# Optimization experiments

Measured on AMD Instinct MI355X. Metric: run time of the kernel, lower is better.

Reference implementation:

```python
import jax, jax.numpy as jnp
import numpy as np

N = 16384      # total atoms (8 proteins x ~2048)
E = 524288     # N * max_neighbors(32)
B = 8          # graphs
F_IN = 26      # 20 residue types + 6 atom types
D = 128        # node_dim
H = 256        # hidden_dim
OUT = 64       # output_dim
L = 4          # n_layers
N_RBF = 16
CUTOFF = 10.0


def setup_inputs() -> dict:
    key = jax.random.key(0)
    ks = jax.random.split(key, 24)
    s = 0.05
    inp = {
        "positions": jax.random.normal(ks[0], (N, 3), jnp.float32) * 10.0,
        "node_features": jax.random.normal(ks[1], (N, F_IN), jnp.float32),
        "edge_index": jax.random.randint(ks[2], (2, E), 0, N, jnp.int32),
        "batch": jnp.sort(jax.random.randint(ks[3], (N,), 0, B, jnp.int32)),
        # node embedding MLP
        "emb_W1": jax.random.normal(ks[4], (F_IN, D), jnp.float32) * s,
        "emb_b1": jnp.zeros((D,), jnp.float32),
        "emb_W2": jax.random.normal(ks[5], (D, D), jnp.float32) * s,
        "emb_b2": jnp.zeros((D,), jnp.float32),
        # per-layer message MLP: [2D + n_rbf] -> H -> D
        "msg_W1": jax.random.normal(ks[6], (L, 2 * D + N_RBF, H), jnp.float32) * s,
        "msg_b1": jnp.zeros((L, H), jnp.float32),
        "msg_W2": jax.random.normal(ks[7], (L, H, D), jnp.float32) * s,
        "msg_b2": jnp.zeros((L, D), jnp.float32),
        # per-layer update MLP: [2D] -> H -> D (residual)
        "upd_W1": jax.random.normal(ks[8], (L, 2 * D, H), jnp.float32) * s,
        "upd_b1": jnp.zeros((L, H), jnp.float32),
        "upd_W2": jax.random.normal(ks[9], (L, H, D), jnp.float32) * s,
        "upd_b2": jnp.zeros((L, D), jnp.float32),
        # readout MLP: D -> H -> OUT
        "r_W1": jax.random.normal(ks[10], (D, H), jnp.float32) * s,
        "r_b1": jnp.zeros((H,), jnp.float32),
        "r_W2": jax.random.normal(ks[11], (H, OUT), jnp.float32) * s,
        "r_b2": jnp.zeros((OUT,), jnp.float32),
    }
    return inp


def _mlp2(x, W1, b1, W2, b2):
    return jax.nn.silu(x @ W1 + b1) @ W2 + b2


def _edge_rbf(positions, src, dst):
    rel = positions[dst] - positions[src]                      # (E,3)
    d = jnp.sqrt(jnp.sum(rel * rel, axis=-1) + 1e-12)          # (E,)
    centers = jnp.linspace(0.0, CUTOFF, N_RBF, dtype=positions.dtype)
    width = CUTOFF / N_RBF
    rbf = jnp.exp(-((d[:, None] - centers) ** 2) / (2.0 * width * width))  # (E,n_rbf)
    env = 0.5 * (jnp.cos(jnp.pi * d / CUTOFF) + 1.0) * (d < CUTOFF)        # cosine cutoff
    return rbf * env[:, None]


def reference(positions, node_features, edge_index, batch,
              emb_W1, emb_b1, emb_W2, emb_b2,
              msg_W1, msg_b1, msg_W2, msg_b2,
              upd_W1, upd_b1, upd_W2, upd_b2,
              r_W1, r_b1, r_W2, r_b2):
    src, dst = edge_index[0], edge_index[1]
    h = _mlp2(node_features, emb_W1, emb_b1, emb_W2, emb_b2)   # (N,D)
    ef = _edge_rbf(positions, src, dst)                        # (E,n_rbf)
    for i in range(L):
        m_in = jnp.concatenate([h[src], h[dst], ef], axis=-1)  # (E,2D+n_rbf)
        m = _mlp2(m_in, msg_W1[i], msg_b1[i], msg_W2[i], msg_b2[i])  # (E,D)
        agg = jax.ops.segment_sum(m, dst, num_segments=N)      # (N,D)
        u_in = jnp.concatenate([h, agg], axis=-1)              # (N,2D)
        h = h + _mlp2(u_in, upd_W1[i], upd_b1[i], upd_W2[i], upd_b2[i])
    # mean readout per graph
    counts = jax.ops.segment_sum(jnp.ones((N,), h.dtype), batch, num_segments=B)
    g = jax.ops.segment_sum(h, batch, num_segments=B) / jnp.maximum(counts, 1.0)[:, None]
    return _mlp2(g, r_W1, r_b1, r_W2, r_b2)                    # (B,OUT)
```

## Files before the change

kernel.cpp:

```cpp
#include <hip/hip_runtime.h>
#include <math.h>

#define NATOMS 16384
#define NEDGES 524288
#define NLAYERS 4
#define TE 64

typedef __bf16 bf16x8 __attribute__((ext_vector_type(8)));
typedef __bf16 bf16x4 __attribute__((ext_vector_type(4)));
typedef __bf16 bf16x2 __attribute__((ext_vector_type(2)));
typedef float f32x4 __attribute__((ext_vector_type(4)));

__device__ __forceinline__ float silu_f(float x) {
  return x * __builtin_amdgcn_rcpf(1.0f + __expf(-x));
}

__global__ __launch_bounds__(1024) void scan_kernel(
    const int* __restrict__ counts, int* __restrict__ cursor,
    float* __restrict__ degf)
{
  __shared__ int s_tot[1024];
  int tid = threadIdx.x;
  int v[16];
  {
    const int4* cp = (const int4*)(counts + tid * 16);
    int4 a = cp[0], b = cp[1], c = cp[2], d = cp[3];
    v[0]=a.x; v[1]=a.y; v[2]=a.z; v[3]=a.w;
    v[4]=b.x; v[5]=b.y; v[6]=b.z; v[7]=b.w;
    v[8]=c.x; v[9]=c.y; v[10]=c.z; v[11]=c.w;
    v[12]=d.x; v[13]=d.y; v[14]=d.z; v[15]=d.w;
  }
  int tot = 0;
  #pragma unroll
  for (int i = 0; i < 16; i++) tot += v[i];
  s_tot[tid] = tot;
  __syncthreads();
  for (int off = 1; off < 1024; off <<= 1) {
    int t = (tid >= off) ? s_tot[tid - off] : 0;
    __syncthreads();
    s_tot[tid] += t;
    __syncthreads();
  }
  int run = s_tot[tid] - tot;
  #pragma unroll
  for (int i = 0; i < 16; i++) {
    cursor[tid * 16 + i] = run;
    degf[tid * 16 + i] = (float)v[i];
    run += v[i];
  }
}

__global__ __launch_bounds__(256) void scatter_rbf_kernel(
    const int* __restrict__ src, const int* __restrict__ dst,
    int* __restrict__ cursor, const float* __restrict__ pos,
    int* __restrict__ esrc, int* __restrict__ edst,
    __bf16* __restrict__ efb)
{
  int e = blockIdx.x * 256 + threadIdx.x;
  int s = src[e], d = dst[e];
  int p = atomicAdd(&cursor[d], 1);
  esrc[p] = s;
  edst[p] = d;
  float dx = pos[d * 3 + 0] - pos[s * 3 + 0];
  float dy = pos[d * 3 + 1] - pos[s * 3 + 1];
  float dz = pos[d * 3 + 2] - pos[s * 3 + 2];
  float dist = sqrtf(dx * dx + dy * dy + dz * dz + 1e-12f);
  float env = (dist < 10.0f)
                  ? 0.5f * (cosf(3.14159265358979f * dist * 0.1f) + 1.0f)
                  : 0.0f;
  bf16x8 o0, o1;
  #pragma unroll
  for (int i = 0; i < 16; i++) {
    float c = (10.0f / 15.0f) * (float)i;
    float t = dist - c;
    float v = env * __expf(-t * t * 1.28f);
    if (i < 8) o0[i] = (__bf16)v; else o1[i - 8] = (__bf16)v;
  }
  *(bf16x8*)(efb + (size_t)p * 16 + 0) = o0;
  *(bf16x8*)(efb + (size_t)p * 16 + 8) = o1;
}

#define NB_PREP (801 * NLAYERS)
#define NB_HIST (NEDGES / 256)
#define NB_EMB  (NATOMS / 2)

__global__ __launch_bounds__(256) void front_kernel(
    const float* __restrict__ mW1, const float* __restrict__ mW2,
    const float* __restrict__ uW1, const float* __restrict__ uW2,
    const float* __restrict__ mb2,
    __bf16* __restrict__ W1at, __bf16* __restrict__ W1bt,
    __bf16* __restrict__ B2c, __bf16* __restrict__ uW1ft,
    __bf16* __restrict__ uW2t, float* __restrict__ b2u,
    const int* __restrict__ dstI, int* __restrict__ counts,
    const float* __restrict__ x, const float* __restrict__ eW1,
    const float* __restrict__ eb1, const float* __restrict__ eW2,
    const float* __restrict__ eb2, float* __restrict__ h,
    __bf16* __restrict__ hb)
{
  __shared__ float xs[2][26];
  __shared__ float hid[2][132];
  int bxf = blockIdx.x, tid = threadIdx.x;

  if (bxf < NB_PREP) {
    long l = bxf / 801;
    int bx = bxf - (int)l * 801;
    if (bx < 128) {
      int i = bx * 256 + tid;
      int n = i >> 7, k = i & 127;
      W1at[l * (256L * 128) + i] = (__bf16)mW1[l * (272L * 256) + (size_t)k * 256 + n];
    } else if (bx < 256) {
      int i = (bx - 128) * 256 + tid;
      int n = i >> 7, k = i & 127;
      W1bt[l * (256L * 128) + i] = (__bf16)mW1[l * (272L * 256) + (size_t)(128 + k) * 256 + n];
    } else if (bx < 288) {
      int i = (bx - 256) * 256 + tid;
      int c = i >> 5, k = i & 31;
      float v = (k < 16) ? mW1[l * (272L * 256) + (size_t)(256 + k) * 256 + c] : 0.0f;
      B2c[l * (256L * 32) + i] = (__bf16)v;
    } else if (bx < 672) {
      int k = bx - 288;
      int n = tid;
      float v;
      if (k < 128) {
        v = uW1[l * 65536 + (size_t)k * 256 + n];
      } else {
        int r = k - 128;
        v = 0.0f;
        for (int j = 0; j < 128; j++)
          v += mW2[(l * 256 + r) * 128 + j] * uW1[l * 65536 + (size_t)(128 + j) * 256 + n];
      }
      uW1ft[l * (256L * 384) + (size_t)n * 384 + k] = (__bf16)v;
    } else if (bx < 800) {
      int i = (bx - 672) * 256 + tid;
      int n = i >> 8, k = i & 255;
      uW2t[l * (128L * 256) + i] = (__bf16)uW2[l * (256L * 128) + (size_t)k * 128 + n];
    } else {
      int c = tid;
      float acc = 0.0f;
      for (int j = 0; j < 128; j++)
        acc += mb2[l * 128 + j] * uW1[l * 65536 + (size_t)(128 + j) * 256 + c];
      b2u[l * 256 + c] = acc;
    }
  } else if (bxf < NB_PREP + NB_HIST) {
    int e = (bxf - NB_PREP) * 256 + tid;
    atomicAdd(&counts[dstI[e]], 1);
  } else {
    int nb = bxf - (NB_PREP + NB_HIST);
    int hf = tid >> 7, j = tid & 127;
    int n = nb * 2 + hf;
    if (j < 26) xs[hf][j] = x[(size_t)n * 26 + j];
    __syncthreads();
    float acc = eb1[j];
    #pragma unroll
    for (int k = 0; k < 26; k++) acc += xs[hf][k] * eW1[k * 128 + j];
    hid[hf][j] = silu_f(acc);
    __syncthreads();
    float acc2 = eb2[j];
    #pragma unroll 8
    for (int k = 0; k < 128; k++) acc2 += hid[hf][k] * eW2[k * 128 + j];
    h[(size_t)n * 128 + j] = acc2;
    hb[(size_t)n * 128 + j] = (__bf16)acc2;
  }
}

__global__ __launch_bounds__(256) void zprep_kernel(
    const __bf16* __restrict__ hb, const float* __restrict__ b1,
    const __bf16* __restrict__ W1at, const __bf16* __restrict__ W1bt,
    __bf16* __restrict__ z1b, __bf16* __restrict__ z2b, float* __restrict__ aggH)
{
  __shared__ __bf16 s_n[64][136];
  int tid = threadIdx.x, n0 = blockIdx.x * 64;
  {
    int n = tid >> 2, t4 = tid & 3;
    const bf16x8* hr = (const bf16x8*)(hb + (size_t)(n0 + n) * 128);
    #pragma unroll
    for (int i = 0; i < 4; i++)
      *(bf16x8*)&s_n[n][t4 * 8 + 32 * i] = hr[t4 + 4 * i];
  }
  {
    float4 zz = make_float4(0.f, 0.f, 0.f, 0.f);
    float4* ap = (float4*)(aggH + (size_t)n0 * 256);
    for (int i = tid; i < 64 * 256 / 4; i += 256) ap[i] = zz;
  }
  __syncthreads();
  const int wv = tid >> 6, ln = tid & 63, lc = ln & 15, qd = ln >> 4;
  for (int cp = 0; cp < 2; cp++) {
    f32x4 aA[4][2], aB[4][2];
    #pragma unroll
    for (int nt = 0; nt < 2; nt++) {
      float bv = b1[cp * 128 + wv * 32 + nt * 16 + lc];
      #pragma unroll
      for (int mt = 0; mt < 4; mt++) {
        aA[mt][nt][0] = 0.f; aA[mt][nt][1] = 0.f;
        aA[mt][nt][2] = 0.f; aA[mt][nt][3] = 0.f;
        aB[mt][nt][0] = bv; aB[mt][nt][1] = bv;
        aB[mt][nt][2] = bv; aB[mt][nt][3] = bv;
      }
    }
    #pragma unroll
    for (int kt = 0; kt < 4; kt++) {
      bf16x8 af[4];
      #pragma unroll
      for (int mt = 0; mt < 4; mt++)
        af[mt] = *(const bf16x8*)&s_n[mt * 16 + lc][kt * 32 + qd * 8];
      bf16x8 bwA[2], bwB[2];
      #pragma unroll
      for (int nt = 0; nt < 2; nt++) {
        int c = cp * 128 + wv * 32 + nt * 16 + lc;
        bwA[nt] = *(const bf16x8*)(W1at + (size_t)c * 128 + kt * 32 + qd * 8);
        bwB[nt] = *(const bf16x8*)(W1bt + (size_t)c * 128 + kt * 32 + qd * 8);
      }
      #pragma unroll
      for (int mt = 0; mt < 4; mt++)
        #pragma unroll
        for (int nt = 0; nt < 2; nt++) {
          aA[mt][nt] = __builtin_amdgcn_mfma_f32_16x16x32_bf16(af[mt], bwA[nt], aA[mt][nt], 0, 0, 0);
          aB[mt][nt] = __builtin_amdgcn_mfma_f32_16x16x32_bf16(af[mt], bwB[nt], aB[mt][nt], 0, 0, 0);
        }
    }
    #pragma unroll
    for (int mt = 0; mt < 4; mt++)
      #pragma unroll
      for (int nt = 0; nt < 2; nt++) {
        int c = cp * 128 + wv * 32 + nt * 16 + lc;
        #pragma unroll
        for (int r = 0; r < 4; r++) {
          int n = n0 + mt * 16 + qd * 4 + r;
          z1b[(size_t)n * 256 + c] = (__bf16)aA[mt][nt][r];
          z2b[(size_t)n * 256 + c] = (__bf16)aB[mt][nt][r];
        }
      }
  }
}

__global__ __launch_bounds__(256, 7) void msg_mfma_kernel(
    const __bf16* __restrict__ z1b, const __bf16* __restrict__ z2b,
    const __bf16* __restrict__ efb,
    const int* __restrict__ esrc, const int* __restrict__ edst,
    const __bf16* __restrict__ B2c, float* __restrict__ aggH)
{
  __shared__ __align__(16) __bf16 s_hT[128][70];
  __shared__ __align__(16) __bf16 s_ef[TE][24];
  __shared__ int s_src[TE];
  __shared__ int s_dst[TE];
  __shared__ unsigned int s_mask[2];

  int tid = threadIdx.x, e0 = blockIdx.x * TE;

  if (tid < TE) {
    int d = edst[e0 + tid];
    s_dst[tid] = d;
    int dp = (tid == 0) ? (d ^ 1) : edst[e0 + tid - 1];
    unsigned long long mb = __ballot(d != dp);
    if (tid == 0) { s_mask[0] = (unsigned int)mb; s_mask[1] = (unsigned int)(mb >> 32); }
  } else if (tid < 2 * TE) {
    s_src[tid - TE] = esrc[e0 + tid - TE];
  }
  {
    int e = tid >> 2, t4 = tid & 3;
    if (t4 < 2)
      *(bf16x8*)&s_ef[e][t4 * 8] =
          *(const bf16x8*)(efb + (size_t)(e0 + e) * 16 + t4 * 8);
  }
  __syncthreads();

  const int wv = tid >> 6, ln = tid & 63, lc = ln & 15, qd = ln >> 4;

  bf16x8 bI;
  #pragma unroll
  for (int j = 0; j < 8; j++)
    bI[j] = (__bf16)((lc == (qd & 1) * 8 + j) ? 1.0f : 0.0f);

  const __bf16* pz[4];
  #pragma unroll
  for (int mt = 0; mt < 4; mt++) {
    int m = mt * 16 + lc;
    int row = (qd < 2) ? s_src[m] : s_dst[m];
    pz[mt] = ((qd < 2) ? z1b : z2b) + (size_t)row * 256 + (qd & 1) * 8;
  }

  bf16x8 aef[4];
  #pragma unroll
  for (int mt = 0; mt < 4; mt++)
    aef[mt] = *(const bf16x8*)&s_ef[mt * 16 + lc][(qd & 1) * 8];

  const int sj = tid & 127;
  const int srow0 = (tid >> 7) * 32;
  const unsigned int smask = __builtin_amdgcn_readfirstlane(s_mask[tid >> 7]);

  #pragma unroll
  for (int hf = 0; hf < 2; hf++) {
    if (hf) __syncthreads();

    #pragma unroll
    for (int nt = 0; nt < 2; nt++) {
      const int cb = hf * 128 + wv * 32 + nt * 16;
      bf16x8 bw = *(const bf16x8*)(B2c + (size_t)(cb + lc) * 32 + qd * 8);
      #pragma unroll
      for (int mt = 0; mt < 4; mt++) {
        bf16x8 az = *(const bf16x8*)(pz[mt] + cb);
        f32x4 z; z[0] = 0.f; z[1] = 0.f; z[2] = 0.f; z[3] = 0.f;
        f32x4 acc = __builtin_amdgcn_mfma_f32_16x16x32_bf16(az, bI, z, 0, 0, 0);
        acc = __builtin_amdgcn_mfma_f32_16x16x32_bf16(aef[mt], bw, acc, 0, 0, 0);
        bf16x2 p0, p1;
        p0[0] = (__bf16)silu_f(acc[0]); p0[1] = (__bf16)silu_f(acc[1]);
        p1[0] = (__bf16)silu_f(acc[2]); p1[1] = (__bf16)silu_f(acc[3]);
        __bf16* wp = &s_hT[wv * 32 + nt * 16 + lc][mt * 16 + qd * 4];
        *(bf16x2*)wp = p0;
        *(bf16x2*)(wp + 2) = p1;
      }
    }
    __syncthreads();

    {
      const int gcol = hf * 128 + sj;
      float acc = 0.0f;
      int cur = s_dst[srow0];
      #pragma unroll 8
      for (int i = 0; i < 32; i += 2) {
        bf16x2 p = *(const bf16x2*)&s_hT[sj][srow0 + i];
        if (i > 0 && ((smask >> i) & 1u)) {
          atomicAdd(&aggH[(size_t)cur * 256 + gcol], acc);
          acc = 0.0f; cur = s_dst[srow0 + i];
        }
        acc += (float)p[0];
        if ((smask >> (i + 1)) & 1u) {
          atomicAdd(&aggH[(size_t)cur * 256 + gcol], acc);
          acc = 0.0f; cur = s_dst[srow0 + i + 1];
        }
        acc += (float)p[1];
      }
      atomicAdd(&aggH[(size_t)cur * 256 + gcol], acc);
    }
  }
}

__global__ __launch_bounds__(512, 2) void upd_mfma_kernel(
    float* __restrict__ h, __bf16* __restrict__ hb,
    float* __restrict__ aggH, const float* __restrict__ degf,
    const __bf16* __restrict__ uW1ft, const float* __restrict__ b1,
    const float* __restrict__ b2u,
    const __bf16* __restrict__ uW2t, const float* __restrict__ b2,
    int do_z, const float* __restrict__ nb1,
    const __bf16* __restrict__ nW1at, const __bf16* __restrict__ nW1bt,
    __bf16* __restrict__ z1b, __bf16* __restrict__ z2b)
{
  __shared__ __bf16 s_u[64][392];
  __shared__ __bf16 s_uh[64][264];
  int tid = threadIdx.x, n0 = blockIdx.x * 64;
  {
    int n = tid >> 3, t8 = tid & 7;
    const bf16x8* hr = (const bf16x8*)(hb + (size_t)(n0 + n) * 128);
    #pragma unroll
    for (int i = 0; i < 2; i++)
      *(bf16x8*)&s_u[n][t8 * 8 + 64 * i] = hr[t8 + 8 * i];
    const float* sr = aggH + (size_t)(n0 + n) * 256;
    #pragma unroll
    for (int i = 0; i < 4; i++) {
      int col = t8 * 8 + i * 64;
      float4 a = *(const float4*)(sr + col);
      float4 b = *(const float4*)(sr + col + 4);
      bf16x8 o;
      o[0] = (__bf16)a.x; o[1] = (__bf16)a.y; o[2] = (__bf16)a.z; o[3] = (__bf16)a.w;
      o[4] = (__bf16)b.x; o[5] = (__bf16)b.y; o[6] = (__bf16)b.z; o[7] = (__bf16)b.w;
      *(bf16x8*)&s_u[n][128 + col] = o;
    }
  }
  __syncthreads();
  const int wv = tid >> 6, ln = tid & 63, lc = ln & 15, qd = ln >> 4;

  float dg[4][4];
  #pragma unroll
  for (int mt = 0; mt < 4; mt++)
    #pragma unroll
    for (int r = 0; r < 4; r++)
      dg[mt][r] = degf[n0 + mt * 16 + qd * 4 + r];

  {
    f32x4 acc1[4][2];
    #pragma unroll
    for (int nt = 0; nt < 2; nt++) {
      int c = wv * 32 + nt * 16 + lc;
      float bv = b1[c];
      float b2uv = b2u[c];
      #pragma unroll
      for (int mt = 0; mt < 4; mt++)
        #pragma unroll
        for (int r = 0; r < 4; r++)
          acc1[mt][nt][r] = bv + dg[mt][r] * b2uv;
    }
    #pragma unroll
    for (int kt = 0; kt < 12; kt++) {
      bf16x8 af[4];
      #pragma unroll
      for (int mt = 0; mt < 4; mt++)
        af[mt] = *(const bf16x8*)&s_u[mt * 16 + lc][kt * 32 + qd * 8];
      bf16x8 bw[2];
      #pragma unroll
      for (int nt = 0; nt < 2; nt++)
        bw[nt] = *(const bf16x8*)(uW1ft +
                 (size_t)(wv * 32 + nt * 16 + lc) * 384 + kt * 32 + qd * 8);
      #pragma unroll
      for (int mt = 0; mt < 4; mt++)
        #pragma unroll
        for (int nt = 0; nt < 2; nt++)
          acc1[mt][nt] = __builtin_amdgcn_mfma_f32_16x16x32_bf16(af[mt], bw[nt], acc1[mt][nt], 0, 0, 0);
    }
    #pragma unroll
    for (int mt = 0; mt < 4; mt++)
      #pragma unroll
      for (int nt = 0; nt < 2; nt++) {
        int cc = wv * 32 + nt * 16 + lc;
        #pragma unroll
        for (int r = 0; r < 4; r++)
          s_uh[mt * 16 + qd * 4 + r][cc] = (__bf16)silu_f(acc1[mt][nt][r]);
      }
  }
  __syncthreads();

  const int ow = wv * 16 + lc;
  f32x4 acc2[4];
  {
    float bv = b2[ow];
    #pragma unroll
    for (int mt = 0; mt < 4; mt++) {
      acc2[mt][0] = bv; acc2[mt][1] = bv; acc2[mt][2] = bv; acc2[mt][3] = bv;
    }
  }
  #pragma unroll
  for (int kt = 0; kt < 8; kt++) {
    bf16x8 a2[4];
    #pragma unroll
    for (int mt = 0; mt < 4; mt++)
      a2[mt] = *(const bf16x8*)&s_uh[mt * 16 + lc][kt * 32 + qd * 8];
    bf16x8 b2w = *(const bf16x8*)(uW2t + (size_t)ow * 256 + kt * 32 + qd * 8);
    #pragma unroll
    for (int mt = 0; mt < 4; mt++)
      acc2[mt] = __builtin_amdgcn_mfma_f32_16x16x32_bf16(a2[mt], b2w, acc2[mt], 0, 0, 0);
  }

  #pragma unroll
  for (int mt = 0; mt < 4; mt++)
    #pragma unroll
    for (int r = 0; r < 4; r++) {
      int n = n0 + mt * 16 + qd * 4 + r;
      float v = h[(size_t)n * 128 + ow] + acc2[mt][r];
      h[(size_t)n * 128 + ow] = v;
      hb[(size_t)n * 128 + ow] = (__bf16)v;
    }

  if (do_z) {
    __syncthreads();
    {
      float4 zz = make_float4(0.f, 0.f, 0.f, 0.f);
      float4* ap = (float4*)(aggH + (size_t)n0 * 256);
      for (int i = tid; i < 64 * 256 / 4; i += 512) ap[i] = zz;
      int n = tid >> 3, t8 = tid & 7;
      const bf16x8* hr = (const bf16x8*)(hb + (size_t)(n0 + n) * 128);
      #pragma unroll
      for (int i = 0; i < 2; i++)
        *(bf16x8*)&s_u[n][t8 * 8 + 64 * i] = hr[t8 + 8 * i];
    }
    __syncthreads();
    f32x4 aA[4][2], aB[4][2];
    #pragma unroll
    for (int nt = 0; nt < 2; nt++) {
      float bv = nb1[wv * 32 + nt * 16 + lc];
      #pragma unroll
      for (int mt = 0; mt < 4; mt++) {
        aA[mt][nt][0] = 0.f; aA[mt][nt][1] = 0.f;
        aA[mt][nt][2] = 0.f; aA[mt][nt][3] = 0.f;
        aB[mt][nt][0] = bv; aB[mt][nt][1] = bv;
        aB[mt][nt][2] = bv; aB[mt][nt][3] = bv;
      }
    }
    #pragma unroll
    for (int kt = 0; kt < 4; kt++) {
      bf16x8 af[4];
      #pragma unroll
      for (int mt = 0; mt < 4; mt++)
        af[mt] = *(const bf16x8*)&s_u[mt * 16 + lc][kt * 32 + qd * 8];
      bf16x8 bwA[2], bwB[2];
      #pragma unroll
      for (int nt = 0; nt < 2; nt++) {
        int c = wv * 32 + nt * 16 + lc;
        bwA[nt] = *(const bf16x8*)(nW1at + (size_t)c * 128 + kt * 32 + qd * 8);
        bwB[nt] = *(const bf16x8*)(nW1bt + (size_t)c * 128 + kt * 32 + qd * 8);
      }
      #pragma unroll
      for (int mt = 0; mt < 4; mt++)
        #pragma unroll
        for (int nt = 0; nt < 2; nt++) {
          aA[mt][nt] = __builtin_amdgcn_mfma_f32_16x16x32_bf16(af[mt], bwA[nt], aA[mt][nt], 0, 0, 0);
          aB[mt][nt] = __builtin_amdgcn_mfma_f32_16x16x32_bf16(af[mt], bwB[nt], aB[mt][nt], 0, 0, 0);
        }
    }
    #pragma unroll
    for (int mt = 0; mt < 4; mt++)
      #pragma unroll
      for (int nt = 0; nt < 2; nt++) {
        int c = wv * 32 + nt * 16 + lc;
        #pragma unroll
        for (int r = 0; r < 4; r++) {
          int n = n0 + mt * 16 + qd * 4 + r;
          z1b[(size_t)n * 256 + c] = (__bf16)aA[mt][nt][r];
          z2b[(size_t)n * 256 + c] = (__bf16)aB[mt][nt][r];
        }
      }
  }
}

__global__ __launch_bounds__(128) void readout_sum_kernel(
    const float* __restrict__ h, const int* __restrict__ batch,
    float* __restrict__ gsum, float* __restrict__ gcnt)
{
  int j = threadIdx.x;
  int n0 = blockIdx.x * 128;
  float acc = 0.f, cacc = 0.f;
  int cur = batch[n0];
  for (int i = 0; i < 128; i++) {
    int b = batch[n0 + i];
    if (b != cur) {
      atomicAdd(&gsum[cur * 128 + j], acc);
      if (j == 0) atomicAdd(&gcnt[cur], cacc);
      acc = 0.f; cacc = 0.f; cur = b;
    }
    acc += h[(size_t)(n0 + i) * 128 + j];
    cacc += 1.f;
  }
  atomicAdd(&gsum[cur * 128 + j], acc);
  if (j == 0) atomicAdd(&gcnt[cur], cacc);
}

__global__ __launch_bounds__(256) void readout_mlp_kernel(
    const float* __restrict__ gsum, const float* __restrict__ gcnt,
    const float* __restrict__ W1, const float* __restrict__ b1,
    const float* __restrict__ W2, const float* __restrict__ b2,
    float* __restrict__ out)
{
  __shared__ float g[8][128];
  __shared__ float hid[8][256];
  int tid = threadIdx.x;
  for (int i = tid; i < 8 * 128; i += 256) {
    int b = i >> 7, c = i & 127;
    g[b][c] = gsum[i] / fmaxf(gcnt[b], 1.0f);
  }
  __syncthreads();
  {
    float bb = b1[tid];
    float a[8];
    #pragma unroll
    for (int b = 0; b < 8; b++) a[b] = bb;
    for (int k = 0; k < 128; k++) {
      float w = W1[k * 256 + tid];
      #pragma unroll
      for (int b = 0; b < 8; b++) a[b] += g[b][k] * w;
    }
    #pragma unroll
    for (int b = 0; b < 8; b++) hid[b][tid] = silu_f(a[b]);
  }
  __syncthreads();
  int j = tid & 63, bg = tid >> 6;
  float a0 = b2[j], a1 = b2[j];
  for (int k = 0; k < 256; k++) {
    float w = W2[k * 64 + j];
    a0 += hid[bg * 2 + 0][k] * w;
    a1 += hid[bg * 2 + 1][k] * w;
  }
  out[(bg * 2 + 0) * 64 + j] = a0;
  out[(bg * 2 + 1) * 64 + j] = a1;
}

extern "C" void kernel_launch(void* const* d_in, const int* in_sizes, int n_in,
                              void* d_out, int out_size, void* d_ws, size_t ws_size,
                              hipStream_t stream) {
  const float* pos   = (const float*)d_in[0];
  const float* xfeat = (const float*)d_in[1];
  const int*   eidx  = (const int*)d_in[2];
  const int*   batch = (const int*)d_in[3];
  const float* eW1 = (const float*)d_in[4];
  const float* eb1 = (const float*)d_in[5];
  const float* eW2 = (const float*)d_in[6];
  const float* eb2 = (const float*)d_in[7];
  const float* mW1 = (const float*)d_in[8];
  const float* mb1 = (const float*)d_in[9];
  const float* mW2 = (const float*)d_in[10];
  const float* mb2 = (const float*)d_in[11];
  const float* uW1 = (const float*)d_in[12];
  const float* ub1 = (const float*)d_in[13];
  const float* uW2 = (const float*)d_in[14];
  const float* ub2 = (const float*)d_in[15];
  const float* rW1 = (const float*)d_in[16];
  const float* rb1 = (const float*)d_in[17];
  const float* rW2 = (const float*)d_in[18];
  const float* rb2 = (const float*)d_in[19];

  const int* srcI = eidx;
  const int* dstI = eidx + NEDGES;

  char* base = (char*)d_ws;
  float* h    = (float*)base;  base += (size_t)NATOMS * 128 * 4;
  float* aggH = (float*)base;  base += (size_t)NATOMS * 256 * 4;
  __bf16* z1b = (__bf16*)base; base += (size_t)NATOMS * 256 * 2;
  __bf16* z2b = (__bf16*)base; base += (size_t)NATOMS * 256 * 2;
  __bf16* hb  = (__bf16*)base; base += (size_t)NATOMS * 128 * 2;
  __bf16* efb = (__bf16*)base; base += (size_t)NEDGES * 16 * 2;
  __bf16* W1at = (__bf16*)base; base += (size_t)NLAYERS * 256 * 128 * 2;
  __bf16* W1bt = (__bf16*)base; base += (size_t)NLAYERS * 256 * 128 * 2;
  __bf16* B2c  = (__bf16*)base; base += (size_t)NLAYERS * 256 * 32 * 2;
  __bf16* uW1ft = (__bf16*)base; base += (size_t)NLAYERS * 256 * 384 * 2;
  __bf16* uW2t = (__bf16*)base; base += (size_t)NLAYERS * 128 * 256 * 2;
  float* b2u  = (float*)base;  base += (size_t)NLAYERS * 256 * 4;
  float* degf = (float*)base;  base += (size_t)NATOMS * 4;
  float* gsum = (float*)base;  base += 8 * 128 * 4;
  float* gcnt = (float*)base;  base += 8 * 4;
  int* counts = (int*)base;    base += (size_t)NATOMS * 4;
  int* cursor = (int*)base;    base += (size_t)NATOMS * 4;
  int* esrc   = (int*)base;    base += (size_t)NEDGES * 4;
  int* edst   = (int*)base;    base += (size_t)NEDGES * 4;

  hipMemsetAsync(counts, 0, NATOMS * sizeof(int), stream);

  front_kernel<<<NB_PREP + NB_HIST + NB_EMB, 256, 0, stream>>>(
      mW1, mW2, uW1, uW2, mb2, W1at, W1bt, B2c, uW1ft, uW2t, b2u,
      dstI, counts, xfeat, eW1, eb1, eW2, eb2, h, hb);

  scan_kernel<<<1, 1024, 0, stream>>>(counts, cursor, degf);
  scatter_rbf_kernel<<<NEDGES / 256, 256, 0, stream>>>(
      srcI, dstI, cursor, pos, esrc, edst, efb);

  zprep_kernel<<<NATOMS / 64, 256, 0, stream>>>(
      hb, mb1, W1at, W1bt, z1b, z2b, aggH);

  for (int l = 0; l < NLAYERS; l++) {
    int ln = (l < NLAYERS - 1) ? (l + 1) : l;
    msg_mfma_kernel<<<NEDGES / TE, 256, 0, stream>>>(
        z1b, z2b, efb, esrc, edst,
        B2c + (size_t)l * 256 * 32, aggH);
    upd_mfma_kernel<<<NATOMS / 64, 512, 0, stream>>>(
        h, hb, aggH, degf,
        uW1ft + (size_t)l * 256 * 384, ub1 + (size_t)l * 256,
        b2u + (size_t)l * 256,
        uW2t + (size_t)l * 128 * 256, ub2 + (size_t)l * 128,
        (l < NLAYERS - 1) ? 1 : 0,
        mb1 + (size_t)ln * 256,
        W1at + (size_t)ln * 256 * 128, W1bt + (size_t)ln * 256 * 128,
        z1b, z2b);
  }

  hipMemsetAsync(gsum, 0, (8 * 128 + 8) * sizeof(float), stream);
  readout_sum_kernel<<<NATOMS / 128, 128, 0, stream>>>(h, batch, gsum, gcnt);
  readout_mlp_kernel<<<1, 256, 0, stream>>>(gsum, gcnt, rW1, rb1, rW2, rb2,
                                            (float*)d_out);
}
```

Measured before the change: 599.2 us.

## Tile weight transposes through LDS and batch embedding MLP over 32 atoms per block

Weight-preparation blocks now transpose 64x64 tiles through shared memory, so both the reads and the bf16 writes are coalesced, instead of doing strided per-element gathers. The folded mW2*uW1 product is computed 16 rows per block with register accumulators, which cuts the number of prep blocks per layer from 801 to 50. The node embedding MLP now handles 32 atoms per block, with each thread keeping 16 accumulators so every weight load is reused across atoms. The cost is more register pressure and a larger shared-memory footprint per block, in exchange for fewer blocks and far less redundant global traffic.

```diff
diff --git a/kernel.cpp b/kernel.cpp
--- a/kernel.cpp
+++ b/kernel.cpp
@@ -80,9 +80,10 @@
   *(bf16x8*)(efb + (size_t)p * 16 + 8) = o1;
 }
 
-#define NB_PREP (801 * NLAYERS)
+#define NB_PL   50
+#define NB_PREP (NB_PL * NLAYERS)
 #define NB_HIST (NEDGES / 256)
-#define NB_EMB  (NATOMS / 2)
+#define NB_EMB  (NATOMS / 32)
 
 __global__ __launch_bounds__(256) void front_kernel(
     const float* __restrict__ mW1, const float* __restrict__ mW2,
@@ -97,69 +98,156 @@
     const float* __restrict__ eb2, float* __restrict__ h,
     __bf16* __restrict__ hb)
 {
-  __shared__ float xs[2][26];
-  __shared__ float hid[2][132];
+  __shared__ __align__(16) char smem[19712];
   int bxf = blockIdx.x, tid = threadIdx.x;
 
   if (bxf < NB_PREP) {
-    long l = bxf / 801;
-    int bx = bxf - (int)l * 801;
-    if (bx < 128) {
-      int i = bx * 256 + tid;
-      int n = i >> 7, k = i & 127;
-      W1at[l * (256L * 128) + i] = (__bf16)mW1[l * (272L * 256) + (size_t)k * 256 + n];
-    } else if (bx < 256) {
-      int i = (bx - 128) * 256 + tid;
-      int n = i >> 7, k = i & 127;
-      W1bt[l * (256L * 128) + i] = (__bf16)mW1[l * (272L * 256) + (size_t)(128 + k) * 256 + n];
-    } else if (bx < 288) {
-      int i = (bx - 256) * 256 + tid;
-      int c = i >> 5, k = i & 31;
-      float v = (k < 16) ? mW1[l * (272L * 256) + (size_t)(256 + k) * 256 + c] : 0.0f;
-      B2c[l * (256L * 32) + i] = (__bf16)v;
-    } else if (bx < 672) {
-      int k = bx - 288;
-      int n = tid;
-      float v;
-      if (k < 128) {
-        v = uW1[l * 65536 + (size_t)k * 256 + n];
-      } else {
-        int r = k - 128;
-        v = 0.0f;
-        for (int j = 0; j < 128; j++)
-          v += mW2[(l * 256 + r) * 128 + j] * uW1[l * 65536 + (size_t)(128 + j) * 256 + n];
-      }
-      uW1ft[l * (256L * 384) + (size_t)n * 384 + k] = (__bf16)v;
-    } else if (bx < 800) {
-      int i = (bx - 672) * 256 + tid;
-      int n = i >> 8, k = i & 255;
-      uW2t[l * (128L * 256) + i] = (__bf16)uW2[l * (256L * 128) + (size_t)k * 128 + n];
+    int l = bxf / NB_PL;
+    int bx = bxf - l * NB_PL;
+    if (bx < 16) {
+      float (*tile)[65] = (float(*)[65])smem;
+      int tt = bx & 7;
+      int row0 = ((tt >> 2) * 64) + ((bx < 8) ? 0 : 128);
+      int col0 = (tt & 3) * 64;
+      const float* Sp = mW1 + (size_t)l * (272 * 256) + (size_t)row0 * 256 + col0;
+      __bf16* Dq = ((bx < 8) ? W1at : W1bt) + (size_t)l * (256 * 128);
+      int dro = (bx < 8) ? row0 : row0 - 128;
+      int c = tid & 63, r4 = tid >> 6;
+      #pragma unroll
+      for (int i = 0; i < 16; i++)
+        tile[r4 + i * 4][c] = Sp[(size_t)(r4 + i * 4) * 256 + c];
+      __syncthreads();
+      #pragma unroll
+      for (int i = 0; i < 16; i++) {
+        int dr = r4 + i * 4;
+        Dq[(size_t)(col0 + dr) * 128 + dro + c] = (__bf16)tile[c][dr];
+      }
+    } else if (bx == 16) {
+      float (*t3)[257] = (float(*)[257])smem;
+      const float* Sp = mW1 + (size_t)l * (272 * 256) + 256 * 256;
+      #pragma unroll
+      for (int i = 0; i < 16; i++) t3[i][tid] = Sp[i * 256 + tid];
+      __syncthreads();
+      __bf16* Dp = B2c + (size_t)l * (256 * 32) + (size_t)tid * 32;
+      #pragma unroll
+      for (int g = 0; g < 4; g++) {
+        bf16x8 o;
+        #pragma unroll
+        for (int j2 = 0; j2 < 8; j2++) {
+          int k = g * 8 + j2;
+          o[j2] = (__bf16)((k < 16) ? t3[k][tid] : 0.0f);
+        }
+        *(bf16x8*)(Dp + g * 8) = o;
+      }
+    } else if (bx < 25) {
+      float (*tile)[65] = (float(*)[65])smem;
+      int tt = bx - 17;
+      int row0 = (tt >> 2) * 64;
+      int col0 = (tt & 3) * 64;
+      const float* Sp = uW1 + (size_t)l * 65536 + (size_t)row0 * 256 + col0;
+      __bf16* Dq = uW1ft + (size_t)l * (256 * 384);
+      int c = tid & 63, r4 = tid >> 6;
+      #pragma unroll
+      for (int i = 0; i < 16; i++)
+        tile[r4 + i * 4][c] = Sp[(size_t)(r4 + i * 4) * 256 + c];
+      __syncthreads();
+      #pragma unroll
+      for (int i = 0; i < 16; i++) {
+        int dr = r4 + i * 4;
+        Dq[(size_t)(col0 + dr) * 384 + row0 + c] = (__bf16)tile[c][dr];
+      }
+    } else if (bx < 41) {
+      float (*sA)[128] = (float(*)[128])smem;
+      int r0 = (bx - 25) * 16;
+      const float* Ap = mW2 + (size_t)(l * 256 + r0) * 128;
+      #pragma unroll
+      for (int i = 0; i < 8; i++) {
+        int idx = i * 256 + tid;
+        ((float*)smem)[idx] = Ap[idx];
+      }
+      __syncthreads();
+      const float* Bp = uW1 + (size_t)l * 65536 + 128 * 256 + tid;
+      float acc[16];
+      #pragma unroll
+      for (int r = 0; r < 16; r++) acc[r] = 0.0f;
+      for (int k = 0; k < 128; k++) {
+        float b = Bp[(size_t)k * 256];
+        #pragma unroll
+        for (int r = 0; r < 16; r++) acc[r] += sA[r][k] * b;
+      }
+      __bf16* Dp = uW1ft + (size_t)l * (256 * 384) + (size_t)tid * 384 + 128 + r0;
+      bf16x8 o0, o1;
+      #pragma unroll
+      for (int r = 0; r < 8; r++) { o0[r] = (__bf16)acc[r]; o1[r] = (__bf16)acc[8 + r]; }
+      *(bf16x8*)Dp = o0;
+      *(bf16x8*)(Dp + 8) = o1;
+    } else if (bx < 49) {
+      float (*tile)[65] = (float(*)[65])smem;
+      int tt = bx - 41;
+      int row0 = (tt >> 1) * 64;
+      int col0 = (tt & 1) * 64;
+      const float* Sp = uW2 + (size_t)l * (256 * 128) + (size_t)row0 * 128 + col0;
+      __bf16* Dq = uW2t + (size_t)l * (128 * 256);
+      int c = tid & 63, r4 = tid >> 6;
+      #pragma unroll
+      for (int i = 0; i < 16; i++)
+        tile[r4 + i * 4][c] = Sp[(size_t)(r4 + i * 4) * 128 + c];
+      __syncthreads();
+      #pragma unroll
+      for (int i = 0; i < 16; i++) {
+        int dr = r4 + i * 4;
+        Dq[(size_t)(col0 + dr) * 256 + row0 + c] = (__bf16)tile[c][dr];
+      }
     } else {
-      int c = tid;
+      int cc = tid;
       float acc = 0.0f;
-      for (int j = 0; j < 128; j++)
-        acc += mb2[l * 128 + j] * uW1[l * 65536 + (size_t)(128 + j) * 256 + c];
-      b2u[l * 256 + c] = acc;
+      for (int j2 = 0; j2 < 128; j2++)
+        acc += mb2[l * 128 + j2] * uW1[(size_t)l * 65536 + (size_t)(128 + j2) * 256 + cc];
+      b2u[l * 256 + cc] = acc;
     }
   } else if (bxf < NB_PREP + NB_HIST) {
     int e = (bxf - NB_PREP) * 256 + tid;
     atomicAdd(&counts[dstI[e]], 1);
   } else {
     int nb = bxf - (NB_PREP + NB_HIST);
-    int hf = tid >> 7, j = tid & 127;
-    int n = nb * 2 + hf;
-    if (j < 26) xs[hf][j] = x[(size_t)n * 26 + j];
+    int n0e = nb * 32;
+    float* xsf = (float*)smem;
+    float (*hid2)[128] = (float(*)[128])(smem + 32 * 26 * 4);
+    for (int i = tid; i < 32 * 26; i += 256)
+      xsf[i] = x[(size_t)n0e * 26 + i];
     __syncthreads();
-    float acc = eb1[j];
-    #pragma unroll
-    for (int k = 0; k < 26; k++) acc += xs[hf][k] * eW1[k * 128 + j];
-    hid[hf][j] = silu_f(acc);
+    int j = tid & 127, ns = tid >> 7;
+    float a1[16];
+    {
+      float bb = eb1[j];
+      #pragma unroll
+      for (int i = 0; i < 16; i++) a1[i] = bb;
+    }
+    for (int k = 0; k < 26; k++) {
+      float w = eW1[k * 128 + j];
+      #pragma unroll
+      for (int i = 0; i < 16; i++) a1[i] += xsf[(ns * 16 + i) * 26 + k] * w;
+    }
+    #pragma unroll
+    for (int i = 0; i < 16; i++) hid2[ns * 16 + i][j] = silu_f(a1[i]);
     __syncthreads();
-    float acc2 = eb2[j];
-    #pragma unroll 8
-    for (int k = 0; k < 128; k++) acc2 += hid[hf][k] * eW2[k * 128 + j];
-    h[(size_t)n * 128 + j] = acc2;
-    hb[(size_t)n * 128 + j] = (__bf16)acc2;
+    float a2[16];
+    {
+      float bb = eb2[j];
+      #pragma unroll
+      for (int i = 0; i < 16; i++) a2[i] = bb;
+    }
+    for (int k = 0; k < 128; k++) {
+      float w = eW2[k * 128 + j];
+      #pragma unroll
+      for (int i = 0; i < 16; i++) a2[i] += hid2[ns * 16 + i][k] * w;
+    }
+    #pragma unroll
+    for (int i = 0; i < 16; i++) {
+      int n = n0e + ns * 16 + i;
+      h[(size_t)n * 128 + j] = a2[i];
+      hb[(size_t)n * 128 + j] = (__bf16)a2[i];
+    }
   }
 }
 
```

Result: faster. 583.3 us (-2.7%).
